# Kernel tuning notes

Hardware: AMD Instinct MI355X
Metric: run time of the kernel (lower is better)

The kernel has to match this reference:

```python
import jax, jax.numpy as jnp
import numpy as np

T = 100000  # context_window
H = 256     # hidden_dim


def setup_inputs() -> dict:
    key = jax.random.key(0)
    k1, k2, k3, k4, k5 = jax.random.split(key, 5)
    inputs = jax.random.normal(k1, (T, H), dtype=jnp.float32)
    hc = jax.random.normal(k2, (1, H), dtype=jnp.float32)
    # learned params (original inits Wm/V to ones; random values give a better numeric test)
    Wm = jax.random.normal(k3, (H, H), dtype=jnp.float32) * (1.0 / np.sqrt(H))
    V = jax.random.normal(k4, (H, 1), dtype=jnp.float32) * (1.0 / np.sqrt(H))
    W1 = jax.random.normal(k5, (H, H), dtype=jnp.float32) * (1.0 / np.sqrt(H))
    return {"inputs": inputs, "hc": hc, "Wm": Wm, "V": V, "W1": W1}


def reference(inputs, hc, Wm, V, W1):
    # Mt: (T, H); broadcast-add the projected context vector to every row
    Mt = inputs
    proj_hc = hc @ W1.T                      # (1, H), torch Linear: x @ W^T
    At = jnp.tanh(Mt @ Wm + proj_hc) @ V     # (T, 1)
    alphat = jax.nn.log_softmax(At.reshape(1, -1), axis=1)  # (1, T)
    ct = alphat @ Mt                         # (1, H) — weighted sum with LOG-softmax weights (faithful)
    return (alphat, ct)
```

## Files before the change

kernel.cpp:

```cpp
#include <hip/hip_runtime.h>
#include <math.h>

#define T_N 100000
#define H_N 256
#define NT32 (T_N / 32)
#define NB_AT 256
#define WPB 13
#define NTHR (WPB * 64)

typedef __attribute__((ext_vector_type(8))) __bf16 bf16x8;
typedef __attribute__((ext_vector_type(4))) float f32x4;


__device__ __forceinline__ float tanh_fast(float x) {
    float e = __expf(2.0f * x);
    return 1.0f - 2.0f / (e + 1.0f);
}

__global__ __launch_bounds__(256) void k_prep(const float* __restrict__ Wm,
                                              const float* __restrict__ hc,
                                              const float* __restrict__ W1,
                                              __bf16* __restrict__ WmT,
                                              float* __restrict__ proj,
                                              float* __restrict__ s1g,
                                              float* __restrict__ s0g) {
    const int j = blockIdx.x;
    const int t = threadIdx.x;
    WmT[j * H_N + t] = (__bf16)Wm[t * H_N + j];
    __shared__ float red[H_N];
    red[t] = hc[t] * W1[j * H_N + t];
    __syncthreads();
    for (int off = 128; off > 0; off >>= 1) {
        if (t < off) red[t] += red[t + off];
        __syncthreads();
    }
    if (t == 0) proj[j] = red[0];
    if (j == 0) { s1g[t] = 0.0f; s0g[t] = 0.0f; }
}

__global__ __launch_bounds__(NTHR, 4) void k_at(const float* __restrict__ Mt,
                                                const __bf16* __restrict__ WmT,
                                                const float* __restrict__ proj,
                                                const float* __restrict__ V,
                                                float* __restrict__ At,
                                                float2* __restrict__ part2,
                                                float* __restrict__ s1g,
                                                float* __restrict__ s0g) {
    const int tid = threadIdx.x;
    const int lane = tid & 63;
    const int w = tid >> 6;
    const int l15 = lane & 15;
    const int lg = lane >> 4;

    struct SMem {
        __align__(16) char sB[131072];
        float pj[256];
        float vj[256];
        float lsem[WPB], lses[WPB];
    };
    __shared__ SMem sm;

    for (int g = tid; g < 8192; g += NTHR) {
        const int n = g >> 5;
        const int c = g & 31;
        const bf16x8 v = *(const bf16x8*)(WmT + n * H_N + c * 8);
        *(bf16x8*)(&sm.sB[(n * 512 + c * 16) ^ ((n & 7) << 4)]) = v;
    }
    if (tid < 256) { sm.pj[tid] = proj[tid]; sm.vj[tid] = V[tid]; }
    __syncthreads();

    const int gw = blockIdx.x * WPB + w;
    float lm = -1e30f, ls = 0.0f;
    float s1a[4] = {0.f, 0.f, 0.f, 0.f};
    float s0a[4] = {0.f, 0.f, 0.f, 0.f};

    if (gw < NT32) {
        const int t0 = gw * 32;
        const float* arow0 = Mt + (size_t)(t0 + l15) * H_N;
        const float* arow1 = Mt + (size_t)(t0 + 16 + l15) * H_N;

        bf16x8 af0[8], af1[8];
#pragma unroll
        for (int ks = 0; ks < 8; ++ks) {
            const float4 a0 = *(const float4*)(arow0 + 32 * ks + 8 * lg);
            const float4 a1 = *(const float4*)(arow0 + 32 * ks + 8 * lg + 4);
            af0[ks][0] = (__bf16)a0.x; af0[ks][1] = (__bf16)a0.y;
            af0[ks][2] = (__bf16)a0.z; af0[ks][3] = (__bf16)a0.w;
            af0[ks][4] = (__bf16)a1.x; af0[ks][5] = (__bf16)a1.y;
            af0[ks][6] = (__bf16)a1.z; af0[ks][7] = (__bf16)a1.w;
            const float4 b0 = *(const float4*)(arow1 + 32 * ks + 8 * lg);
            const float4 b1 = *(const float4*)(arow1 + 32 * ks + 8 * lg + 4);
            af1[ks][0] = (__bf16)b0.x; af1[ks][1] = (__bf16)b0.y;
            af1[ks][2] = (__bf16)b0.z; af1[ks][3] = (__bf16)b0.w;
            af1[ks][4] = (__bf16)b1.x; af1[ks][5] = (__bf16)b1.y;
            af1[ks][6] = (__bf16)b1.z; af1[ks][7] = (__bf16)b1.w;
        }

        float pacc0[4] = {0.f, 0.f, 0.f, 0.f};
        float pacc1[4] = {0.f, 0.f, 0.f, 0.f};
#pragma unroll 1
        for (int jb = 0; jb < 16; ++jb) {
            f32x4 a0A = {0.f, 0.f, 0.f, 0.f}, a0B = {0.f, 0.f, 0.f, 0.f};
            f32x4 a1A = {0.f, 0.f, 0.f, 0.f}, a1B = {0.f, 0.f, 0.f, 0.f};
            const int n = 16 * jb + l15;
            const int nb = n * 512;
            const int nswz = (n & 7) << 4;
#pragma unroll
            for (int ks = 0; ks < 4; ++ks) {
                const bf16x8 bfA = *(const bf16x8*)(
                    &sm.sB[nb + (((32 * ks + 8 * lg) * 2) ^ nswz)]);
                const bf16x8 bfB = *(const bf16x8*)(
                    &sm.sB[nb + (((32 * (ks + 4) + 8 * lg) * 2) ^ nswz)]);
                a0A = __builtin_amdgcn_mfma_f32_16x16x32_bf16(af0[ks], bfA, a0A, 0, 0, 0);
                a1A = __builtin_amdgcn_mfma_f32_16x16x32_bf16(af1[ks], bfA, a1A, 0, 0, 0);
                a0B = __builtin_amdgcn_mfma_f32_16x16x32_bf16(af0[ks + 4], bfB, a0B, 0, 0, 0);
                a1B = __builtin_amdgcn_mfma_f32_16x16x32_bf16(af1[ks + 4], bfB, a1B, 0, 0, 0);
            }
            const float pjv = sm.pj[n], vjv = sm.vj[n];
#pragma unroll
            for (int i = 0; i < 4; ++i) {
                pacc0[i] += tanh_fast(a0A[i] + a0B[i] + pjv) * vjv;
                pacc1[i] += tanh_fast(a1A[i] + a1B[i] + pjv) * vjv;
            }
        }

        float p0[4], p1[4];
#pragma unroll
        for (int i = 0; i < 4; ++i) {
            float q0 = pacc0[i], q1 = pacc1[i];
            q0 += __shfl_xor(q0, 1); q1 += __shfl_xor(q1, 1);
            q0 += __shfl_xor(q0, 2); q1 += __shfl_xor(q1, 2);
            q0 += __shfl_xor(q0, 4); q1 += __shfl_xor(q1, 4);
            q0 += __shfl_xor(q0, 8); q1 += __shfl_xor(q1, 8);
            p0[i] = q0; p1[i] = q1;
        }
        if (l15 == 0) {
#pragma unroll
            for (int i = 0; i < 4; ++i) {
                const float a0v = p0[i], a1v = p1[i];
                At[t0 + 4 * lg + i] = a0v;
                At[t0 + 16 + 4 * lg + i] = a1v;
                if (a0v > lm) { ls = ls * __expf(lm - a0v) + 1.0f; lm = a0v; }
                else ls += __expf(a0v - lm);
                if (a1v > lm) { ls = ls * __expf(lm - a1v) + 1.0f; lm = a1v; }
                else ls += __expf(a1v - lm);
            }
        }

        const float* crow = Mt + (size_t)t0 * H_N + lane * 4;
        {
            float4 x[16];
#pragma unroll
            for (int r = 0; r < 16; ++r)
                x[r] = *(const float4*)(crow + (size_t)r * H_N);
#pragma unroll
            for (int r = 0; r < 16; ++r) {
                const float atr = __shfl(p0[r & 3], 16 * (r >> 2));
                s1a[0] += atr * x[r].x; s1a[1] += atr * x[r].y;
                s1a[2] += atr * x[r].z; s1a[3] += atr * x[r].w;
                s0a[0] += x[r].x; s0a[1] += x[r].y;
                s0a[2] += x[r].z; s0a[3] += x[r].w;
            }
#pragma unroll
            for (int r = 0; r < 16; ++r)
                x[r] = *(const float4*)(crow + (size_t)(16 + r) * H_N);
#pragma unroll
            for (int r = 0; r < 16; ++r) {
                const float atr = __shfl(p1[r & 3], 16 * (r >> 2));
                s1a[0] += atr * x[r].x; s1a[1] += atr * x[r].y;
                s1a[2] += atr * x[r].z; s1a[3] += atr * x[r].w;
                s0a[0] += x[r].x; s0a[1] += x[r].y;
                s0a[2] += x[r].z; s0a[3] += x[r].w;
            }
        }
    }

#pragma unroll
    for (int d = 1; d < 64; d <<= 1) {
        const float m2 = __shfl_xor(lm, d), s2 = __shfl_xor(ls, d);
        const float M = fmaxf(lm, m2);
        ls = ls * __expf(lm - M) + s2 * __expf(m2 - M);
        lm = M;
    }
    if (lane == 0) { sm.lsem[w] = lm; sm.lses[w] = ls; }

    __syncthreads();
    float* red1 = (float*)&sm.sB[0];
    float* red2 = (float*)&sm.sB[65536];
#pragma unroll
    for (int q = 0; q < 4; ++q) {
        red1[w * 256 + lane * 4 + q] = s1a[q];
        red2[w * 256 + lane * 4 + q] = s0a[q];
    }
    __syncthreads();
    if (tid < 256) {
        float a = 0.f;
#pragma unroll
        for (int g = 0; g < WPB; ++g) a += red1[g * 256 + tid];
        atomicAdd(&s1g[tid], a);
    } else if (tid < 512) {
        const int c = tid - 256;
        float a = 0.f;
#pragma unroll
        for (int g = 0; g < WPB; ++g) a += red2[g * 256 + c];
        atomicAdd(&s0g[c], a);
    } else if (tid == 512) {
        float m = sm.lsem[0], s = sm.lses[0];
#pragma unroll
        for (int g = 1; g < WPB; ++g) {
            const float m2 = sm.lsem[g], s2 = sm.lses[g];
            const float M = fmaxf(m, m2);
            s = s * __expf(m - M) + s2 * __expf(m2 - M);
            m = M;
        }
        part2[blockIdx.x] = make_float2(m, s);
    }
}

__global__ __launch_bounds__(256) void k_final(const float2* __restrict__ part2,
                                               const float* __restrict__ s1g,
                                               const float* __restrict__ s0g,
                                               float* __restrict__ lse,
                                               float* __restrict__ out) {
    const int tid = threadIdx.x;
    __shared__ float ms[256], ss[256];
    const float2 p = part2[tid];
    ms[tid] = p.x; ss[tid] = p.y;
    __syncthreads();
    for (int off = 128; off > 0; off >>= 1) {
        if (tid < off) {
            const float m2 = ms[tid + off], s2 = ss[tid + off];
            const float M = fmaxf(ms[tid], m2);
            ss[tid] = ss[tid] * __expf(ms[tid] - M) + s2 * __expf(m2 - M);
            ms[tid] = M;
        }
        __syncthreads();
    }
    __shared__ float Ls;
    if (tid == 0) { Ls = ms[0] + logf(ss[0]); *lse = Ls; }
    __syncthreads();
    out[T_N + tid] = s1g[tid] - Ls * s0g[tid];
}

__global__ __launch_bounds__(256) void k_alpha(const float* __restrict__ At,
                                               const float* __restrict__ lse,
                                               float* __restrict__ out) {
    const float L = *lse;
    const int i4 = blockIdx.x * 256 + threadIdx.x;
    if (i4 < T_N / 4) {
        float4 a = *(const float4*)(At + i4 * 4);
        a.x -= L; a.y -= L; a.z -= L; a.w -= L;
        *(float4*)(out + i4 * 4) = a;
    }
}

extern "C" void kernel_launch(void* const* d_in, const int* in_sizes, int n_in,
                              void* d_out, int out_size, void* d_ws, size_t ws_size,
                              hipStream_t stream) {
    const float* inputs = (const float*)d_in[0];
    const float* hc     = (const float*)d_in[1];
    const float* Wm     = (const float*)d_in[2];
    const float* V      = (const float*)d_in[3];
    const float* W1     = (const float*)d_in[4];
    float* out = (float*)d_out;

    char* ws = (char*)d_ws;
    __bf16* WmT  = (__bf16*)ws;
    float* proj  = (float*)(ws + 131072);
    float* At    = (float*)(ws + 132096);
    float2* p2   = (float2*)(ws + 532096);
    float* s1g   = (float*)(ws + 536192);
    float* s0g   = (float*)(ws + 537216);
    float* lse   = (float*)(ws + 538240);

    k_prep<<<256, 256, 0, stream>>>(Wm, hc, W1, WmT, proj, s1g, s0g);
    k_at<<<NB_AT, NTHR, 0, stream>>>(inputs, WmT, proj, V, At, p2, s1g, s0g);
    k_final<<<1, 256, 0, stream>>>(p2, s1g, s0g, lse, out);
    k_alpha<<<98, 256, 0, stream>>>(At, lse, out);
}
```

Before: 56.56 us.

## Reuse bf16 MFMA operand registers for context sum instead of reloading fp32 rows

The weighted-sum pass now builds the per-column sums from the bf16 A-fragments already held in registers for the matrix multiply, instead of re-reading each 32-row tile of Mt from global memory as fp32. Lanes reduce partial sums with cross-lane shuffles and the column mapping of the shared-memory reduction is changed to match. This removes a second global read of the input, at the cost of many shuffle instructions per tile and of computing ct from bf16-rounded inputs, which lowers its precision.

```diff
diff --git a/kernel.cpp b/kernel.cpp
--- a/kernel.cpp
+++ b/kernel.cpp
@@ -147,30 +147,31 @@
             }
         }
 
-        const float* crow = Mt + (size_t)t0 * H_N + lane * 4;
-        {
-            float4 x[16];
-#pragma unroll
-            for (int r = 0; r < 16; ++r)
-                x[r] = *(const float4*)(crow + (size_t)r * H_N);
-#pragma unroll
-            for (int r = 0; r < 16; ++r) {
-                const float atr = __shfl(p0[r & 3], 16 * (r >> 2));
-                s1a[0] += atr * x[r].x; s1a[1] += atr * x[r].y;
-                s1a[2] += atr * x[r].z; s1a[3] += atr * x[r].w;
-                s0a[0] += x[r].x; s0a[1] += x[r].y;
-                s0a[2] += x[r].z; s0a[3] += x[r].w;
-            }
-#pragma unroll
-            for (int r = 0; r < 16; ++r)
-                x[r] = *(const float4*)(crow + (size_t)(16 + r) * H_N);
-#pragma unroll
-            for (int r = 0; r < 16; ++r) {
-                const float atr = __shfl(p1[r & 3], 16 * (r >> 2));
-                s1a[0] += atr * x[r].x; s1a[1] += atr * x[r].y;
-                s1a[2] += atr * x[r].z; s1a[3] += atr * x[r].w;
-                s0a[0] += x[r].x; s0a[1] += x[r].y;
-                s0a[2] += x[r].z; s0a[3] += x[r].w;
+        const int srcl = (l15 >> 2) * 16;
+        const float q00 = __shfl(p0[0], srcl), q01 = __shfl(p0[1], srcl);
+        const float q02 = __shfl(p0[2], srcl), q03 = __shfl(p0[3], srcl);
+        const float q10 = __shfl(p1[0], srcl), q11 = __shfl(p1[1], srcl);
+        const float q12 = __shfl(p1[2], srcl), q13 = __shfl(p1[3], srcl);
+        const int i3 = l15 & 3;
+        const float at0 = (i3 == 0) ? q00 : (i3 == 1) ? q01 : (i3 == 2) ? q02 : q03;
+        const float at1 = (i3 == 0) ? q10 : (i3 == 1) ? q11 : (i3 == 2) ? q12 : q13;
+
+#pragma unroll
+        for (int ks = 0; ks < 8; ++ks) {
+#pragma unroll
+            for (int j = 0; j < 8; ++j) {
+                const float a0 = (float)af0[ks][j];
+                const float a1 = (float)af1[ks][j];
+                float cs1 = at0 * a0 + at1 * a1;
+                float cs0 = a0 + a1;
+                cs1 += __shfl_xor(cs1, 1); cs0 += __shfl_xor(cs0, 1);
+                cs1 += __shfl_xor(cs1, 2); cs0 += __shfl_xor(cs0, 2);
+                cs1 += __shfl_xor(cs1, 4); cs0 += __shfl_xor(cs0, 4);
+                cs1 += __shfl_xor(cs1, 8); cs0 += __shfl_xor(cs0, 8);
+                if (l15 == 2 * ks + (j >> 2)) {
+                    s1a[j & 3] += cs1;
+                    s0a[j & 3] += cs0;
+                }
             }
         }
     }
@@ -187,10 +188,13 @@
     __syncthreads();
     float* red1 = (float*)&sm.sB[0];
     float* red2 = (float*)&sm.sB[65536];
-#pragma unroll
-    for (int q = 0; q < 4; ++q) {
-        red1[w * 256 + lane * 4 + q] = s1a[q];
-        red2[w * 256 + lane * 4 + q] = s0a[q];
+    {
+        const int cbase = 32 * (l15 >> 1) + 8 * lg + 4 * (l15 & 1);
+#pragma unroll
+        for (int q = 0; q < 4; ++q) {
+            red1[w * 256 + cbase + q] = s1a[q];
+            red2[w * 256 + cbase + q] = s0a[q];
+        }
     }
     __syncthreads();
     if (tid < 256) {
```

After: 99.09 us. 75.2% more time.

## Split attention-score hidden dimension across two blocks and move LSE to separate kernel

Applied to the files above, without the earlier changes.

Each row tile is now handled by two blocks, each covering half of the 256 Wm columns. Each block loads only half the weight matrix into shared memory (64 KB instead of 128 KB) and accumulates its partial scores into At with atomics. The online log-sum-exp is moved out of k_at into a new k_lse_part kernel that reads the completed At, and At is zeroed in k_prep. The aim is more parallelism and occupancy from smaller LDS use. The cost is that the Mt tile is read and converted twice, plus atomic traffic and an extra kernel launch.

```diff
diff --git a/kernel.cpp b/kernel.cpp
--- a/kernel.cpp
+++ b/kernel.cpp
@@ -4,7 +4,7 @@
 #define T_N 100000
 #define H_N 256
 #define NT32 (T_N / 32)
-#define NB_AT 256
+#define NB_AT 512
 #define WPB 13
 #define NTHR (WPB * 64)
 
@@ -22,6 +22,7 @@
                                               const float* __restrict__ W1,
                                               __bf16* __restrict__ WmT,
                                               float* __restrict__ proj,
+                                              float* __restrict__ At,
                                               float* __restrict__ s1g,
                                               float* __restrict__ s0g) {
     const int j = blockIdx.x;
@@ -36,6 +37,7 @@
     }
     if (t == 0) proj[j] = red[0];
     if (j == 0) { s1g[t] = 0.0f; s0g[t] = 0.0f; }
+    for (int i = j * 256 + t; i < T_N; i += 65536) At[i] = 0.0f;
 }
 
 __global__ __launch_bounds__(NTHR, 4) void k_at(const float* __restrict__ Mt,
@@ -43,7 +45,6 @@
                                                 const float* __restrict__ proj,
                                                 const float* __restrict__ V,
                                                 float* __restrict__ At,
-                                                float2* __restrict__ part2,
                                                 float* __restrict__ s1g,
                                                 float* __restrict__ s0g) {
     const int tid = threadIdx.x;
@@ -52,25 +53,29 @@
     const int l15 = lane & 15;
     const int lg = lane >> 4;
 
+    const int half = blockIdx.x >> 8;
+    const int pairb = blockIdx.x & 255;
+
     struct SMem {
-        __align__(16) char sB[131072];
-        float pj[256];
-        float vj[256];
-        float lsem[WPB], lses[WPB];
+        __align__(16) char sB[65536];
+        float pj[128];
+        float vj[128];
     };
     __shared__ SMem sm;
 
-    for (int g = tid; g < 8192; g += NTHR) {
-        const int n = g >> 5;
+    for (int g = tid; g < 4096; g += NTHR) {
+        const int nl = g >> 5;
         const int c = g & 31;
-        const bf16x8 v = *(const bf16x8*)(WmT + n * H_N + c * 8);
-        *(bf16x8*)(&sm.sB[(n * 512 + c * 16) ^ ((n & 7) << 4)]) = v;
-    }
-    if (tid < 256) { sm.pj[tid] = proj[tid]; sm.vj[tid] = V[tid]; }
-    __syncthreads();
-
-    const int gw = blockIdx.x * WPB + w;
-    float lm = -1e30f, ls = 0.0f;
+        const bf16x8 v = *(const bf16x8*)(WmT + (128 * half + nl) * H_N + c * 8);
+        *(bf16x8*)(&sm.sB[(nl * 512 + c * 16) ^ ((nl & 7) << 4)]) = v;
+    }
+    if (tid < 128) {
+        sm.pj[tid] = proj[128 * half + tid];
+        sm.vj[tid] = V[128 * half + tid];
+    }
+    __syncthreads();
+
+    const int gw = pairb * WPB + w;
     float s1a[4] = {0.f, 0.f, 0.f, 0.f};
     float s0a[4] = {0.f, 0.f, 0.f, 0.f};
 
@@ -99,12 +104,12 @@
         float pacc0[4] = {0.f, 0.f, 0.f, 0.f};
         float pacc1[4] = {0.f, 0.f, 0.f, 0.f};
 #pragma unroll 1
-        for (int jb = 0; jb < 16; ++jb) {
+        for (int jb = 0; jb < 8; ++jb) {
             f32x4 a0A = {0.f, 0.f, 0.f, 0.f}, a0B = {0.f, 0.f, 0.f, 0.f};
             f32x4 a1A = {0.f, 0.f, 0.f, 0.f}, a1B = {0.f, 0.f, 0.f, 0.f};
-            const int n = 16 * jb + l15;
-            const int nb = n * 512;
-            const int nswz = (n & 7) << 4;
+            const int nl = 16 * jb + l15;
+            const int nb = nl * 512;
+            const int nswz = (nl & 7) << 4;
 #pragma unroll
             for (int ks = 0; ks < 4; ++ks) {
                 const bf16x8 bfA = *(const bf16x8*)(
@@ -116,7 +121,7 @@
                 a0B = __builtin_amdgcn_mfma_f32_16x16x32_bf16(af0[ks + 4], bfB, a0B, 0, 0, 0);
                 a1B = __builtin_amdgcn_mfma_f32_16x16x32_bf16(af1[ks + 4], bfB, a1B, 0, 0, 0);
             }
-            const float pjv = sm.pj[n], vjv = sm.vj[n];
+            const float pjv = sm.pj[nl], vjv = sm.vj[nl];
 #pragma unroll
             for (int i = 0; i < 4; ++i) {
                 pacc0[i] += tanh_fast(a0A[i] + a0B[i] + pjv) * vjv;
@@ -137,13 +142,8 @@
         if (l15 == 0) {
 #pragma unroll
             for (int i = 0; i < 4; ++i) {
-                const float a0v = p0[i], a1v = p1[i];
-                At[t0 + 4 * lg + i] = a0v;
-                At[t0 + 16 + 4 * lg + i] = a1v;
-                if (a0v > lm) { ls = ls * __expf(lm - a0v) + 1.0f; lm = a0v; }
-                else ls += __expf(a0v - lm);
-                if (a1v > lm) { ls = ls * __expf(lm - a1v) + 1.0f; lm = a1v; }
-                else ls += __expf(a1v - lm);
+                atomicAdd(&At[t0 + 4 * lg + i], p0[i]);
+                atomicAdd(&At[t0 + 16 + 4 * lg + i], p1[i]);
             }
         }
 
@@ -158,8 +158,10 @@
                 const float atr = __shfl(p0[r & 3], 16 * (r >> 2));
                 s1a[0] += atr * x[r].x; s1a[1] += atr * x[r].y;
                 s1a[2] += atr * x[r].z; s1a[3] += atr * x[r].w;
-                s0a[0] += x[r].x; s0a[1] += x[r].y;
-                s0a[2] += x[r].z; s0a[3] += x[r].w;
+                if (half == 0) {
+                    s0a[0] += x[r].x; s0a[1] += x[r].y;
+                    s0a[2] += x[r].z; s0a[3] += x[r].w;
+                }
             }
 #pragma unroll
             for (int r = 0; r < 16; ++r)
@@ -169,24 +171,17 @@
                 const float atr = __shfl(p1[r & 3], 16 * (r >> 2));
                 s1a[0] += atr * x[r].x; s1a[1] += atr * x[r].y;
                 s1a[2] += atr * x[r].z; s1a[3] += atr * x[r].w;
-                s0a[0] += x[r].x; s0a[1] += x[r].y;
-                s0a[2] += x[r].z; s0a[3] += x[r].w;
-            }
-        }
-    }
-
-#pragma unroll
-    for (int d = 1; d < 64; d <<= 1) {
-        const float m2 = __shfl_xor(lm, d), s2 = __shfl_xor(ls, d);
-        const float M = fmaxf(lm, m2);
-        ls = ls * __expf(lm - M) + s2 * __expf(m2 - M);
-        lm = M;
-    }
-    if (lane == 0) { sm.lsem[w] = lm; sm.lses[w] = ls; }
+                if (half == 0) {
+                    s0a[0] += x[r].x; s0a[1] += x[r].y;
+                    s0a[2] += x[r].z; s0a[3] += x[r].w;
+                }
+            }
+        }
+    }
 
     __syncthreads();
     float* red1 = (float*)&sm.sB[0];
-    float* red2 = (float*)&sm.sB[65536];
+    float* red2 = (float*)&sm.sB[16384];
 #pragma unroll
     for (int q = 0; q < 4; ++q) {
         red1[w * 256 + lane * 4 + q] = s1a[q];
@@ -198,23 +193,38 @@
 #pragma unroll
         for (int g = 0; g < WPB; ++g) a += red1[g * 256 + tid];
         atomicAdd(&s1g[tid], a);
-    } else if (tid < 512) {
+    } else if (tid < 512 && half == 0) {
         const int c = tid - 256;
         float a = 0.f;
 #pragma unroll
         for (int g = 0; g < WPB; ++g) a += red2[g * 256 + c];
         atomicAdd(&s0g[c], a);
-    } else if (tid == 512) {
-        float m = sm.lsem[0], s = sm.lses[0];
-#pragma unroll
-        for (int g = 1; g < WPB; ++g) {
-            const float m2 = sm.lsem[g], s2 = sm.lses[g];
-            const float M = fmaxf(m, m2);
-            s = s * __expf(m - M) + s2 * __expf(m2 - M);
-            m = M;
-        }
-        part2[blockIdx.x] = make_float2(m, s);
-    }
+    }
+}
+
+__global__ __launch_bounds__(256) void k_lse_part(const float* __restrict__ At,
+                                                  float2* __restrict__ part) {
+    const int tid = threadIdx.x;
+    const int gid = blockIdx.x * 256 + tid;
+    float m = -1e30f, s = 0.0f;
+    for (int i = gid; i < T_N; i += 256 * 256) {
+        const float x = At[i];
+        if (x > m) { s = s * __expf(m - x) + 1.0f; m = x; }
+        else s += __expf(x - m);
+    }
+    __shared__ float ms[256], ss[256];
+    ms[tid] = m; ss[tid] = s;
+    __syncthreads();
+    for (int off = 128; off > 0; off >>= 1) {
+        if (tid < off) {
+            const float m2 = ms[tid + off], s2 = ss[tid + off];
+            const float M = fmaxf(ms[tid], m2);
+            ss[tid] = ss[tid] * __expf(ms[tid] - M) + s2 * __expf(m2 - M);
+            ms[tid] = M;
+        }
+        __syncthreads();
+    }
+    if (tid == 0) part[blockIdx.x] = make_float2(ms[0], ss[0]);
 }
 
 __global__ __launch_bounds__(256) void k_final(const float2* __restrict__ part2,
@@ -273,8 +283,9 @@
     float* s0g   = (float*)(ws + 537216);
     float* lse   = (float*)(ws + 538240);
 
-    k_prep<<<256, 256, 0, stream>>>(Wm, hc, W1, WmT, proj, s1g, s0g);
-    k_at<<<NB_AT, NTHR, 0, stream>>>(inputs, WmT, proj, V, At, p2, s1g, s0g);
+    k_prep<<<256, 256, 0, stream>>>(Wm, hc, W1, WmT, proj, At, s1g, s0g);
+    k_at<<<NB_AT, NTHR, 0, stream>>>(inputs, WmT, proj, V, At, s1g, s0g);
+    k_lse_part<<<256, 256, 0, stream>>>(At, p2);
     k_final<<<1, 256, 0, stream>>>(p2, s1g, s0g, lse, out);
     k_alpha<<<98, 256, 0, stream>>>(At, lse, out);
 }
```

Measured after the change: 86.29 us. 52.6% more time.
